# Optimization experiments

Hardware: AMD Instinct MI355X
Metric: run time of the kernel (lower is better)

The kernel has to match this reference:

```python
import jax, jax.numpy as jnp
import numpy as np

N = 50000
E = 800000
DIM_H = 128
EPS = 1e-5


def _glorot(key, shape):
    fan_in, fan_out = shape[0], shape[1]
    lim = np.sqrt(6.0 / (fan_in + fan_out))
    return jax.random.uniform(key, shape, jnp.float32, -lim, lim)


def setup_inputs() -> dict:
    key = jax.random.key(0)
    ks = jax.random.split(key, 12)
    h = jax.random.normal(ks[0], (N, DIM_H), jnp.float32)
    x = jax.random.normal(ks[1], (N, 3), jnp.float32)
    e = jax.random.randint(ks[2], (2, E), 0, N, jnp.int32)
    dx = jax.random.normal(ks[3], (E, 3), jnp.float32)
    d2 = jax.random.uniform(ks[4], (E, 1), jnp.float32)
    # message_layer.phi params: Linear(2*dim_h+1, dim_h), LayerNorm(dim_h), Linear(dim_h, dim_h)
    W1 = _glorot(ks[5], (2 * DIM_H + 1, DIM_H))
    b1 = jnp.zeros((DIM_H,), jnp.float32)
    g1 = jnp.ones((DIM_H,), jnp.float32)
    beta1 = jnp.zeros((DIM_H,), jnp.float32)
    W2 = _glorot(ks[6], (DIM_H, DIM_H))
    b2 = jnp.zeros((DIM_H,), jnp.float32)
    # outer phi params: Linear(dim_h, dim_h), Linear(dim_h, 1)
    W3 = _glorot(ks[7], (DIM_H, DIM_H))
    b3 = jnp.zeros((DIM_H,), jnp.float32)
    W4 = _glorot(ks[8], (DIM_H, 1))
    b4 = jnp.zeros((1,), jnp.float32)
    return {"h": h, "x": x, "e": e, "dx": dx, "d2": d2,
            "W1": W1, "b1": b1, "g1": g1, "beta1": beta1,
            "W2": W2, "b2": b2, "W3": W3, "b3": b3, "W4": W4, "b4": b4}


def _layernorm(z, g, b):
    mu = jnp.mean(z, axis=-1, keepdims=True)
    var = jnp.mean(jnp.square(z - mu), axis=-1, keepdims=True)
    return (z - mu) * jax.lax.rsqrt(var + EPS) * g + b


def reference(h, x, e, dx, d2, W1, b1, g1, beta1, W2, b2, W3, b3, W4, b4):
    ei, ej = e[0], e[1]
    hi = h[ei]                      # [E, dim_h]
    hj = h[ej]                      # [E, dim_h]
    msg = jnp.concatenate((hi, hj, d2), axis=-1)   # [E, 2*dim_h+1]
    msg = jax.nn.silu(msg @ W1 + b1)
    msg = _layernorm(msg, g1, beta1)
    msg = jax.nn.silu(msg @ W2 + b2)               # [E, dim_h]
    scale = jax.nn.silu(msg @ W3 + b3) @ W4 + b4   # [E, 1]
    vec = dx * scale                               # [E, 3]
    agg = jax.ops.segment_sum(vec, ei, num_segments=N)  # [N, 3]
    return x + agg
```

## Files before the change

### kernel.cpp

```cpp
#include <hip/hip_runtime.h>
#include <hip/hip_bf16.h>
#include <cstdint>

#define NN 50000
#define NE 800000
#define DH 128
#define TILES 50000

typedef __bf16 bf16;
typedef __bf16 bf16x8 __attribute__((ext_vector_type(8)));
typedef float  f32x4  __attribute__((ext_vector_type(4)));

__device__ __forceinline__ float fast_silu(float x) {
    float e = __expf(-x);
    return x * __builtin_amdgcn_rcpf(1.0f + e);
}

__global__ void prep_kernel(const float* __restrict__ W1, const float* __restrict__ W2,
                            const float* __restrict__ W3, const float* __restrict__ b1,
                            const float* __restrict__ g1, const float* __restrict__ bt1,
                            const float* __restrict__ b2, const float* __restrict__ b3,
                            const float* __restrict__ W4,
                            bf16* __restrict__ w1aT, bf16* __restrict__ w1bT,
                            bf16* __restrict__ w2T,  bf16* __restrict__ w3T,
                            float* __restrict__ smalls) {
    int i = blockIdx.x * 256 + threadIdx.x;
    int n = i >> 7, k = i & 127;
    w1aT[i] = (bf16)W1[k * DH + n];
    w1bT[i] = (bf16)W1[(k + DH) * DH + n];
    w2T[i]  = (bf16)W2[k * DH + n];
    w3T[i]  = (bf16)W3[k * DH + n];
    if (i < DH) {
        smalls[i]          = W1[256 * DH + i];
        smalls[DH + i]     = b1[i];
        smalls[2 * DH + i] = g1[i];
        smalls[3 * DH + i] = bt1[i];
        smalls[4 * DH + i] = b2[i];
        smalls[5 * DH + i] = b3[i];
        smalls[6 * DH + i] = W4[i];
    }
}

__global__ __launch_bounds__(256) void node_kernel(const float* __restrict__ h,
                                                   const bf16* __restrict__ w1aT,
                                                   const bf16* __restrict__ w1bT,
                                                   bf16* __restrict__ An,
                                                   bf16* __restrict__ Bn) {
    int lane = threadIdx.x & 63, wid = threadIdx.x >> 6;
    int r = lane & 15, g = lane >> 4;
    int wt = blockIdx.x * 4 + wid;
    if (wt >= (NN / 16)) return;
    int base = wt * 16;
    int node = base + r;

    bf16x8 ha[4];
#pragma unroll
    for (int s = 0; s < 4; s++) {
        const float* hp = h + (size_t)node * DH + s * 32 + g * 8;
        float4 p0 = *(const float4*)hp;
        float4 p1 = *(const float4*)(hp + 4);
        ha[s][0] = (bf16)p0.x; ha[s][1] = (bf16)p0.y;
        ha[s][2] = (bf16)p0.z; ha[s][3] = (bf16)p0.w;
        ha[s][4] = (bf16)p1.x; ha[s][5] = (bf16)p1.y;
        ha[s][6] = (bf16)p1.z; ha[s][7] = (bf16)p1.w;
    }
#pragma unroll
    for (int t = 0; t < 16; t++) {
        const bf16* wmat = (t < 8) ? w1aT : w1bT;
        int n = (t & 7) * 16 + r;
        f32x4 acc = {0.f, 0.f, 0.f, 0.f};
#pragma unroll
        for (int s = 0; s < 4; s++) {
            bf16x8 wb = *(const bf16x8*)(wmat + n * DH + s * 32 + g * 8);
            acc = __builtin_amdgcn_mfma_f32_16x16x32_bf16(ha[s], wb, acc, 0, 0, 0);
        }
        bf16* dst = (t < 8) ? An : Bn;
#pragma unroll
        for (int jj = 0; jj < 4; jj++)
            dst[(size_t)(base + g * 4 + jj) * DH + (t & 7) * 16 + r] = (bf16)acc[jj];
    }
}

__global__ void init_kernel(const float* __restrict__ x, float* __restrict__ out, int n) {
    int i = blockIdx.x * 256 + threadIdx.x;
    if (i < n) out[i] = x[i];
}

__global__ __launch_bounds__(512, 2) void edge_kernel(
    const bf16* __restrict__ An, const bf16* __restrict__ Bn,
    const bf16* __restrict__ w2T, const bf16* __restrict__ w3T,
    const float* __restrict__ smalls, const float* __restrict__ b4p,
    const int* __restrict__ e, const float* __restrict__ dxv,
    const float* __restrict__ d2, float* __restrict__ out) {
    __shared__ __align__(16) bf16 sW2[128 * 136];
    __shared__ __align__(16) bf16 sW3[128 * 136];
    __shared__ __align__(16) bf16 sY[8 * 16 * 136];
    __shared__ float sSm[7 * 128];

    int tid = threadIdx.x;
    for (int c = tid; c < 2048; c += 512) {
        int row = c >> 4, col = (c & 15) * 8;
        *(bf16x8*)&sW2[row * 136 + col] = *(const bf16x8*)&w2T[row * 128 + col];
        *(bf16x8*)&sW3[row * 136 + col] = *(const bf16x8*)&w3T[row * 128 + col];
    }
    if (tid < 128) {
#pragma unroll
        for (int a = 0; a < 7; a++) sSm[a * 128 + tid] = smalls[a * 128 + tid];
    }
    __syncthreads();

    const float* s_w1c = sSm;
    const float* s_b1  = sSm + 128;
    const float* s_g1  = sSm + 256;
    const float* s_bt1 = sSm + 384;
    const float* s_b2  = sSm + 512;
    const float* s_b3  = sSm + 640;
    const float* s_W4  = sSm + 768;
    float b4v = b4p[0];

    int lane = tid & 63, wid = tid >> 6;
    int r = lane & 15, g = lane >> 4;
    bf16* yw = &sY[wid * 16 * 136];
    int wgid = blockIdx.x * 8 + wid;
    int nw = gridDim.x * 8;

    for (int tile = wgid; tile < TILES; tile += nw) {
        int base = tile * 16;
        int ei = e[base + r];
        int ej = e[NE + base + r];
        float d2v = d2[base + r];
        const bf16* Ar = An + (size_t)ei * DH;
        const bf16* Br = Bn + (size_t)ej * DH;

        float z[4][8];
#pragma unroll
        for (int s = 0; s < 4; s++) {
            bf16x8 av = *(const bf16x8*)(Ar + s * 32 + g * 8);
            bf16x8 bv = *(const bf16x8*)(Br + s * 32 + g * 8);
#pragma unroll
            for (int j = 0; j < 8; j++) {
                int f = s * 32 + g * 8 + j;
                float zz = (float)av[j] + (float)bv[j] + d2v * s_w1c[f] + s_b1[f];
                z[s][j] = fast_silu(zz);
            }
        }
        float sum = 0.f, sq = 0.f;
#pragma unroll
        for (int s = 0; s < 4; s++)
#pragma unroll
            for (int j = 0; j < 8; j++) { sum += z[s][j]; sq += z[s][j] * z[s][j]; }
        sum += __shfl_xor(sum, 16); sq += __shfl_xor(sq, 16);
        sum += __shfl_xor(sum, 32); sq += __shfl_xor(sq, 32);
        float mu = sum * 0.0078125f;
        float var = sq * 0.0078125f - mu * mu;
        float rs = __builtin_amdgcn_rsqf(var + 1e-5f);

        bf16x8 af[4];
#pragma unroll
        for (int s = 0; s < 4; s++)
#pragma unroll
            for (int j = 0; j < 8; j++) {
                int f = s * 32 + g * 8 + j;
                af[s][j] = (bf16)((z[s][j] - mu) * rs * s_g1[f] + s_bt1[f]);
            }

#pragma unroll
        for (int t = 0; t < 8; t++) {
            f32x4 acc = {0.f, 0.f, 0.f, 0.f};
#pragma unroll
            for (int s = 0; s < 4; s++) {
                bf16x8 wb = *(const bf16x8*)&sW2[(t * 16 + r) * 136 + s * 32 + g * 8];
                acc = __builtin_amdgcn_mfma_f32_16x16x32_bf16(af[s], wb, acc, 0, 0, 0);
            }
            int n = t * 16 + r;
            float b2n = s_b2[n];
#pragma unroll
            for (int jj = 0; jj < 4; jj++)
                yw[(g * 4 + jj) * 136 + n] = (bf16)fast_silu(acc[jj] + b2n);
        }
        bf16x8 a2[4];
#pragma unroll
        for (int s = 0; s < 4; s++)
            a2[s] = *(const bf16x8*)&yw[r * 136 + s * 32 + g * 8];

        float part[4] = {0.f, 0.f, 0.f, 0.f};
#pragma unroll
        for (int t = 0; t < 8; t++) {
            f32x4 acc = {0.f, 0.f, 0.f, 0.f};
#pragma unroll
            for (int s = 0; s < 4; s++) {
                bf16x8 wb = *(const bf16x8*)&sW3[(t * 16 + r) * 136 + s * 32 + g * 8];
                acc = __builtin_amdgcn_mfma_f32_16x16x32_bf16(a2[s], wb, acc, 0, 0, 0);
            }
            int n = t * 16 + r;
            float b3n = s_b3[n], w4n = s_W4[n];
#pragma unroll
            for (int jj = 0; jj < 4; jj++)
                part[jj] += fast_silu(acc[jj] + b3n) * w4n;
        }
#pragma unroll
        for (int jj = 0; jj < 4; jj++) {
            part[jj] += __shfl_xor(part[jj], 1);
            part[jj] += __shfl_xor(part[jj], 2);
            part[jj] += __shfl_xor(part[jj], 4);
            part[jj] += __shfl_xor(part[jj], 8);
        }
#pragma unroll
        for (int jj = 0; jj < 4; jj++) {
            float scale = part[jj] + b4v;
            int m = g * 4 + jj;
            int eim = __shfl(ei, m);
            if (r < 3)
                atomicAdd(&out[(size_t)eim * 3 + r],
                          dxv[(size_t)(base + m) * 3 + r] * scale);
        }
    }
}

extern "C" void kernel_launch(void* const* d_in, const int* in_sizes, int n_in,
                              void* d_out, int out_size, void* d_ws, size_t ws_size,
                              hipStream_t stream) {
    const float* h   = (const float*)d_in[0];
    const float* x   = (const float*)d_in[1];
    const int*   e   = (const int*)d_in[2];
    const float* dxv = (const float*)d_in[3];
    const float* d2  = (const float*)d_in[4];
    const float* W1  = (const float*)d_in[5];
    const float* b1  = (const float*)d_in[6];
    const float* g1  = (const float*)d_in[7];
    const float* bt1 = (const float*)d_in[8];
    const float* W2  = (const float*)d_in[9];
    const float* b2  = (const float*)d_in[10];
    const float* W3  = (const float*)d_in[11];
    const float* b3  = (const float*)d_in[12];
    const float* W4  = (const float*)d_in[13];
    const float* b4  = (const float*)d_in[14];

    char* ws = (char*)d_ws;
    bf16* An    = (bf16*)(ws);
    bf16* Bn    = (bf16*)(ws + 12800000);
    bf16* w1aT  = (bf16*)(ws + 25600000);
    bf16* w1bT  = (bf16*)(ws + 25600000 + 32768);
    bf16* w2T   = (bf16*)(ws + 25600000 + 65536);
    bf16* w3T   = (bf16*)(ws + 25600000 + 98304);
    float* smalls = (float*)(ws + 25600000 + 131072);
    float* out  = (float*)d_out;

    prep_kernel<<<64, 256, 0, stream>>>(W1, W2, W3, b1, g1, bt1, b2, b3, W4,
                                        w1aT, w1bT, w2T, w3T, smalls);
    node_kernel<<<(NN / 16 + 3) / 4, 256, 0, stream>>>(h, w1aT, w1bT, An, Bn);
    init_kernel<<<(NN * 3 + 255) / 256, 256, 0, stream>>>(x, out, NN * 3);
    edge_kernel<<<256, 512, 0, stream>>>(An, Bn, w2T, w3T, smalls, b4,
                                         e, dxv, d2, out);
}
```

Measured before the change: 411.2 us.

## Keep layer-2 output in registers via transposed MFMA and pre-permuted W3

The edge kernel now computes W2·af with weights as the A operand, so the layer-2 output lands in a register layout that feeds the W3 MFMA directly, with no LDS round-trip. W3 is pre-permuted in the prep kernel to match that layout. W2 and W3 are read straight from global/L2 instead of being staged in shared memory, and the b3/W4 vectors are interleaved. LDS use drops sharply, so the grid doubles to 512 blocks, at the cost of repeated global weight loads per tile and an extra register array for acc1.

```diff
diff --git a/kernel.cpp b/kernel.cpp
--- a/kernel.cpp
+++ b/kernel.cpp
@@ -22,22 +22,27 @@
                             const float* __restrict__ b2, const float* __restrict__ b3,
                             const float* __restrict__ W4,
                             bf16* __restrict__ w1aT, bf16* __restrict__ w1bT,
-                            bf16* __restrict__ w2T,  bf16* __restrict__ w3T,
+                            bf16* __restrict__ w2T,  bf16* __restrict__ w3P,
                             float* __restrict__ smalls) {
     int i = blockIdx.x * 256 + threadIdx.x;
     int n = i >> 7, k = i & 127;
     w1aT[i] = (bf16)W1[k * DH + n];
     w1bT[i] = (bf16)W1[(k + DH) * DH + n];
     w2T[i]  = (bf16)W2[k * DH + n];
-    w3T[i]  = (bf16)W3[k * DH + n];
+    {
+        int j = i & 7, l = (i >> 3) & 63, t2 = (i >> 9) & 7, s2 = (i >> 12) & 3;
+        int g = l >> 4, r = l & 15;
+        int n_in = (2 * s2 + (j >> 2)) * 16 + 4 * g + (j & 3);
+        w3P[i] = (bf16)W3[n_in * DH + t2 * 16 + r];
+    }
     if (i < DH) {
-        smalls[i]          = W1[256 * DH + i];
-        smalls[DH + i]     = b1[i];
-        smalls[2 * DH + i] = g1[i];
-        smalls[3 * DH + i] = bt1[i];
-        smalls[4 * DH + i] = b2[i];
-        smalls[5 * DH + i] = b3[i];
-        smalls[6 * DH + i] = W4[i];
+        smalls[i]           = W1[256 * DH + i];
+        smalls[DH + i]      = b1[i];
+        smalls[2 * DH + i]  = g1[i];
+        smalls[3 * DH + i]  = bt1[i];
+        smalls[4 * DH + i]  = b2[i];
+        smalls[896 + 2 * i]     = b3[i];
+        smalls[896 + 2 * i + 1] = W4[i];
     }
 }
 
@@ -88,24 +93,16 @@
 
 __global__ __launch_bounds__(512, 2) void edge_kernel(
     const bf16* __restrict__ An, const bf16* __restrict__ Bn,
-    const bf16* __restrict__ w2T, const bf16* __restrict__ w3T,
+    const bf16* __restrict__ w2T, const bf16* __restrict__ w3P,
     const float* __restrict__ smalls, const float* __restrict__ b4p,
     const int* __restrict__ e, const float* __restrict__ dxv,
     const float* __restrict__ d2, float* __restrict__ out) {
-    __shared__ __align__(16) bf16 sW2[128 * 136];
-    __shared__ __align__(16) bf16 sW3[128 * 136];
-    __shared__ __align__(16) bf16 sY[8 * 16 * 136];
-    __shared__ float sSm[7 * 128];
+    __shared__ float sSm[1152];
 
     int tid = threadIdx.x;
-    for (int c = tid; c < 2048; c += 512) {
-        int row = c >> 4, col = (c & 15) * 8;
-        *(bf16x8*)&sW2[row * 136 + col] = *(const bf16x8*)&w2T[row * 128 + col];
-        *(bf16x8*)&sW3[row * 136 + col] = *(const bf16x8*)&w3T[row * 128 + col];
-    }
     if (tid < 128) {
 #pragma unroll
-        for (int a = 0; a < 7; a++) sSm[a * 128 + tid] = smalls[a * 128 + tid];
+        for (int a = 0; a < 9; a++) sSm[a * 128 + tid] = smalls[a * 128 + tid];
     }
     __syncthreads();
 
@@ -114,13 +111,13 @@
     const float* s_g1  = sSm + 256;
     const float* s_bt1 = sSm + 384;
     const float* s_b2  = sSm + 512;
-    const float* s_b3  = sSm + 640;
-    const float* s_W4  = sSm + 768;
+    const float* s_bw  = sSm + 896;
     float b4v = b4p[0];
 
     int lane = tid & 63, wid = tid >> 6;
     int r = lane & 15, g = lane >> 4;
-    bf16* yw = &sY[wid * 16 * 136];
+    const bf16* w2base = w2T + r * DH + g * 8;
+    const bf16* w3base = w3P + (size_t)lane * 8;
     int wgid = blockIdx.x * 8 + wid;
     int nw = gridDim.x * 8;
 
@@ -164,55 +161,61 @@
                 af[s][j] = (bf16)((z[s][j] - mu) * rs * s_g1[f] + s_bt1[f]);
             }
 
+        f32x4 acc1[8];
 #pragma unroll
         for (int t = 0; t < 8; t++) {
             f32x4 acc = {0.f, 0.f, 0.f, 0.f};
 #pragma unroll
             for (int s = 0; s < 4; s++) {
-                bf16x8 wb = *(const bf16x8*)&sW2[(t * 16 + r) * 136 + s * 32 + g * 8];
-                acc = __builtin_amdgcn_mfma_f32_16x16x32_bf16(af[s], wb, acc, 0, 0, 0);
-            }
-            int n = t * 16 + r;
-            float b2n = s_b2[n];
-#pragma unroll
-            for (int jj = 0; jj < 4; jj++)
-                yw[(g * 4 + jj) * 136 + n] = (bf16)fast_silu(acc[jj] + b2n);
-        }
-        bf16x8 a2[4];
-#pragma unroll
-        for (int s = 0; s < 4; s++)
-            a2[s] = *(const bf16x8*)&yw[r * 136 + s * 32 + g * 8];
-
-        float part[4] = {0.f, 0.f, 0.f, 0.f};
-#pragma unroll
-        for (int t = 0; t < 8; t++) {
+                bf16x8 wa = *(const bf16x8*)(w2base + t * 16 * DH + s * 32);
+                acc = __builtin_amdgcn_mfma_f32_16x16x32_bf16(wa, af[s], acc, 0, 0, 0);
+            }
+            acc1[t] = acc;
+        }
+
+        bf16x8 pb[4];
+#pragma unroll
+        for (int s2 = 0; s2 < 4; s2++) {
+#pragma unroll
+            for (int half = 0; half < 2; half++) {
+                int t = 2 * s2 + half;
+                float4 b2q = *(const float4*)&s_b2[t * 16 + 4 * g];
+#pragma unroll
+                for (int jj = 0; jj < 4; jj++) {
+                    float bq = (jj == 0) ? b2q.x : (jj == 1) ? b2q.y
+                             : (jj == 2) ? b2q.z : b2q.w;
+                    pb[s2][half * 4 + jj] = (bf16)fast_silu(acc1[t][jj] + bq);
+                }
+            }
+        }
+
+        float part = 0.f;
+#pragma unroll
+        for (int t2 = 0; t2 < 8; t2++) {
             f32x4 acc = {0.f, 0.f, 0.f, 0.f};
 #pragma unroll
-            for (int s = 0; s < 4; s++) {
-                bf16x8 wb = *(const bf16x8*)&sW3[(t * 16 + r) * 136 + s * 32 + g * 8];
-                acc = __builtin_amdgcn_mfma_f32_16x16x32_bf16(a2[s], wb, acc, 0, 0, 0);
-            }
-            int n = t * 16 + r;
-            float b3n = s_b3[n], w4n = s_W4[n];
-#pragma unroll
-            for (int jj = 0; jj < 4; jj++)
-                part[jj] += fast_silu(acc[jj] + b3n) * w4n;
-        }
-#pragma unroll
-        for (int jj = 0; jj < 4; jj++) {
-            part[jj] += __shfl_xor(part[jj], 1);
-            part[jj] += __shfl_xor(part[jj], 2);
-            part[jj] += __shfl_xor(part[jj], 4);
-            part[jj] += __shfl_xor(part[jj], 8);
-        }
-#pragma unroll
-        for (int jj = 0; jj < 4; jj++) {
-            float scale = part[jj] + b4v;
-            int m = g * 4 + jj;
+            for (int s2 = 0; s2 < 4; s2++) {
+                bf16x8 wa = *(const bf16x8*)(w3base + (s2 * 8 + t2) * 512);
+                acc = __builtin_amdgcn_mfma_f32_16x16x32_bf16(wa, pb[s2], acc, 0, 0, 0);
+            }
+            float4 p0 = *(const float4*)&s_bw[2 * (t2 * 16 + 4 * g)];
+            float4 p1 = *(const float4*)&s_bw[2 * (t2 * 16 + 4 * g) + 4];
+            part += fast_silu(acc[0] + p0.x) * p0.y;
+            part += fast_silu(acc[1] + p0.z) * p0.w;
+            part += fast_silu(acc[2] + p1.x) * p1.y;
+            part += fast_silu(acc[3] + p1.z) * p1.w;
+        }
+        part += __shfl_xor(part, 16);
+        part += __shfl_xor(part, 32);
+        float scale_r = part + b4v;
+
+        {
+            int m = lane >> 2, c3 = lane & 3;
+            float sc = __shfl(scale_r, m);
             int eim = __shfl(ei, m);
-            if (r < 3)
-                atomicAdd(&out[(size_t)eim * 3 + r],
-                          dxv[(size_t)(base + m) * 3 + r] * scale);
+            if (c3 < 3)
+                atomicAdd(&out[(size_t)eim * 3 + c3],
+                          dxv[(size_t)(base + m) * 3 + c3] * sc);
         }
     }
 }
@@ -237,19 +240,19 @@
     const float* b4  = (const float*)d_in[14];
 
     char* ws = (char*)d_ws;
-    bf16* An    = (bf16*)(ws);
-    bf16* Bn    = (bf16*)(ws + 12800000);
-    bf16* w1aT  = (bf16*)(ws + 25600000);
-    bf16* w1bT  = (bf16*)(ws + 25600000 + 32768);
-    bf16* w2T   = (bf16*)(ws + 25600000 + 65536);
-    bf16* w3T   = (bf16*)(ws + 25600000 + 98304);
-    float* smalls = (float*)(ws + 25600000 + 131072);
-    float* out  = (float*)d_out;
+    bf16* An     = (bf16*)(ws);
+    bf16* Bn     = (bf16*)(ws + 12800000);
+    bf16* w1aT   = (bf16*)(ws + 25600000);
+    bf16* w1bT   = (bf16*)(ws + 25632768);
+    bf16* w2T    = (bf16*)(ws + 25665536);
+    bf16* w3P    = (bf16*)(ws + 25698304);
+    float* smalls = (float*)(ws + 25731072);
+    float* out   = (float*)d_out;
 
     prep_kernel<<<64, 256, 0, stream>>>(W1, W2, W3, b1, g1, bt1, b2, b3, W4,
-                                        w1aT, w1bT, w2T, w3T, smalls);
+                                        w1aT, w1bT, w2T, w3P, smalls);
     node_kernel<<<(NN / 16 + 3) / 4, 256, 0, stream>>>(h, w1aT, w1bT, An, Bn);
     init_kernel<<<(NN * 3 + 255) / 256, 256, 0, stream>>>(x, out, NN * 3);
-    edge_kernel<<<256, 512, 0, stream>>>(An, Bn, w2T, w3T, smalls, b4,
+    edge_kernel<<<512, 512, 0, stream>>>(An, Bn, w2T, w3P, smalls, b4,
                                          e, dxv, d2, out);
 }
```

Measured after the change: 968.2 us. 135% more time.
